# Kernel optimization log

Measured on AMD Instinct MI355X. Metric: run time of the kernel, lower is better.

Reference implementation:

```python
import jax, jax.numpy as jnp
import numpy as np

B, T, HID = 2, 2048, 2048
NH, NKV, D = 16, 4, 128
WIN = 512
ROPE_BASE = 10000.0
SCALE = D ** -0.5
EPS = 1e-12


def setup_inputs() -> dict:
    key = jax.random.key(0)
    ks = jax.random.split(key, 5)
    x = jax.random.normal(ks[0], (B, T, HID), dtype=jnp.float32)
    wq = jax.random.normal(ks[1], (HID, NH * D), dtype=jnp.float32) * 0.02
    wk = jax.random.normal(ks[2], (HID, NKV * D), dtype=jnp.float32) * 0.02
    wv = jax.random.normal(ks[3], (HID, NKV * D), dtype=jnp.float32) * 0.02
    wo = jax.random.normal(ks[4], (NH * D, HID), dtype=jnp.float32) * 0.02
    return {"x": x, "wq": wq, "wk": wk, "wv": wv, "wo": wo}


def _rope_tables(t, offset=0):
    inv_freq = 1.0 / (ROPE_BASE ** (jnp.arange(0, D, 2, dtype=jnp.float32) / D))
    pos = jnp.arange(offset, offset + t, dtype=jnp.float32)
    freqs = pos[:, None] * inv_freq[None, :]              # [t, D/2]
    cos = jnp.concatenate([jnp.cos(freqs), jnp.cos(freqs)], axis=-1)  # [t, D]
    sin = jnp.concatenate([jnp.sin(freqs), jnp.sin(freqs)], axis=-1)
    return cos, sin


def _apply_rope(x, cos, sin):
    # x: [B, H, T, D]; rotate-half formulation
    x1, x2 = jnp.split(x, 2, axis=-1)
    rot = jnp.concatenate([-x2, x1], axis=-1)
    return x * cos[None, None] + rot * sin[None, None]


def _l2norm(x):
    n = jnp.sqrt(jnp.sum(x * x, axis=-1, keepdims=True))
    return x / jnp.maximum(n, EPS)


def _forward(x, wq, wk, wv, wo):
    b, t, _ = x.shape
    q = (x @ wq).reshape(b, t, NH, D).transpose(0, 2, 1, 3)    # [B,H,T,D]
    k = (x @ wk).reshape(b, t, NKV, D).transpose(0, 2, 1, 3)   # [B,Hk,T,D]
    v = (x @ wv).reshape(b, t, NKV, D).transpose(0, 2, 1, 3)
    q = _l2norm(q)
    k = _l2norm(k)
    cos, sin = _rope_tables(t, offset=0)
    q = _apply_rope(q, cos, sin)
    k = _apply_rope(k, cos, sin)
    rep = NH // NKV
    k = jnp.repeat(k, rep, axis=1)                             # GQA repeat_interleave
    v = jnp.repeat(v, rep, axis=1)
    i = jnp.arange(t)
    allowed = (i[None, :] <= i[:, None]) & (i[None, :] > i[:, None] - WIN)  # [T,T]
    logits = jnp.einsum("bhid,bhjd->bhij", q, k) * SCALE
    logits = jnp.where(allowed[None, None], logits, -jnp.inf)
    attn = jax.nn.softmax(logits, axis=-1)
    out = jnp.einsum("bhij,bhjd->bhid", attn, v)
    out = out.transpose(0, 2, 1, 3).reshape(b, t, NH * D)
    return out @ wo


def reference(x, wq, wk, wv, wo):
    return _forward(x, wq, wk, wv, wo)
```

## Files before the change

kernel.cpp:

```cpp
#include <hip/hip_runtime.h>
#include <hip/hip_bf16.h>
#include <cstdint>

#define NHQ 16
#define NKVH 4
#define HDIM 128
#define WINSZ 512
#define TSEQ 2048
#define ATTN_SCALE 0.08838834764831845f

typedef __attribute__((ext_vector_type(8))) short s16x8;
typedef __attribute__((ext_vector_type(4))) float f32x4;

__device__ __forceinline__ void gload16(const void* g, void* lds) {
  __builtin_amdgcn_global_load_lds(
      (const __attribute__((address_space(1))) unsigned int*)g,
      (__attribute__((address_space(3))) unsigned int*)(uintptr_t)lds,
      16, 0, 0);
}

__device__ __forceinline__ f32x4 mfma16(s16x8 a, s16x8 b, f32x4 c) {
  return __builtin_amdgcn_mfma_f32_16x16x32_bf16(a, b, c, 0, 0, 0);
}

#define SBAR() asm volatile("s_barrier" ::: "memory")
#define VMCNT(n) asm volatile("s_waitcnt vmcnt(" #n ")" ::: "memory")
#define LGKM(n) asm volatile("s_waitcnt lgkmcnt(" #n ")" ::: "memory")

__global__ __launch_bounds__(256) void rope_tables_kernel(float* __restrict__ cosT,
                                                          float* __restrict__ sinT) {
  int idx = blockIdx.x * 256 + threadIdx.x;
  int t = idx >> 6, d2 = idx & 63;
  float inv = powf(10000.0f, -(float)d2 / 64.0f);
  float a = (float)t * inv;
  cosT[idx] = cosf(a);
  sinT[idx] = sinf(a);
}

__global__ __launch_bounds__(256) void cast_kernel(const float* __restrict__ in,
                                                   __bf16* __restrict__ out, int n4) {
  int i = blockIdx.x * 256 + threadIdx.x;
  if (i >= n4) return;
  float4 v = ((const float4*)in)[i];
  union { __bf16 h[4]; uint2 u; } pk;
  pk.h[0] = (__bf16)v.x; pk.h[1] = (__bf16)v.y; pk.h[2] = (__bf16)v.z; pk.h[3] = (__bf16)v.w;
  ((uint2*)out)[i] = pk.u;
}

__global__ __launch_bounds__(256) void transpose_cast(const float* __restrict__ in,
                                                      __bf16* __restrict__ out, int R, int C) {
  __shared__ float tile[32][33];
  int c0 = blockIdx.x * 32, r0 = blockIdx.y * 32;
  int tx = threadIdx.x, ty = threadIdx.y;
#pragma unroll
  for (int i = 0; i < 4; i++)
    tile[ty + i * 8][tx] = in[(size_t)(r0 + ty + i * 8) * C + c0 + tx];
  __syncthreads();
#pragma unroll
  for (int i = 0; i < 4; i++)
    out[(size_t)(c0 + ty + i * 8) * R + r0 + tx] = (__bf16)tile[tx][ty + i * 8];
}

__global__ __launch_bounds__(256) void vtrans(const __bf16* __restrict__ V,
                                              __bf16* __restrict__ VT) {
  __shared__ __bf16 t32[32][33];
  int bh = blockIdx.z;
  int t0 = blockIdx.y * 32, d0 = blockIdx.x * 32;
  const __bf16* src = V + (size_t)bh * TSEQ * HDIM;
  __bf16* dst = VT + (size_t)bh * HDIM * TSEQ;
  int tx = threadIdx.x, ty = threadIdx.y;
#pragma unroll
  for (int i = 0; i < 4; i++)
    t32[ty + i * 8][tx] = src[(size_t)(t0 + ty + i * 8) * HDIM + d0 + tx];
  __syncthreads();
#pragma unroll
  for (int i = 0; i < 4; i++)
    dst[(size_t)(d0 + ty + i * 8) * TSEQ + t0 + tx] = t32[tx][ty + i * 8];
}

template <int MODE>
__global__ __launch_bounds__(512, 2) void gemm8(const __bf16* __restrict__ A,
                                                const __bf16* __restrict__ Bt,
                                                float* __restrict__ Cf,
                                                __bf16* __restrict__ Qo, __bf16* __restrict__ Ko,
                                                __bf16* __restrict__ Vo, int M, int N, int K) {
  __shared__ __attribute__((aligned(16))) char Lds[2][65536];

  const int tid = threadIdx.x;
  const int w = tid >> 6, lane = tid & 63;
  const int wm = w >> 2, wn = w & 3;

  const int nbx = gridDim.x;
  const int nwg = nbx * gridDim.y;
  const int bid = blockIdx.y * nbx + blockIdx.x;
  const int q8 = nwg >> 3, r8 = nwg & 7;
  const int xcd = bid & 7, idx = bid >> 3;
  const int swz = (xcd < r8 ? xcd * (q8 + 1) : r8 * (q8 + 1) + (xcd - r8) * q8) + idx;
  const int bx = swz % nbx, by = swz / nbx;
  const int m0 = by * 256, n0 = bx * 256;

  const int ru = tid >> 3;
  const int cs = (tid & 7) ^ (ru & 7);
  const __bf16* gAs = A + (size_t)(m0 + ru) * K + cs * 8;
  const __bf16* gBs = Bt + (size_t)(n0 + ru) * K + cs * 8;

  auto stA = [&](int tt, int u) {
    gload16(gAs + (size_t)(64 * u) * K + tt * 64, Lds[tt & 1] + u * 8192 + w * 1024);
  };
  auto stB = [&](int tt, int u) {
    gload16(gBs + (size_t)(64 * u) * K + tt * 64, Lds[tt & 1] + 32768 + u * 8192 + w * 1024);
  };

  const int rowb = (lane & 15) * 128;
  const int cph0 = (((lane >> 4)) ^ (lane & 7)) * 16;
  const int cph1 = ((4 + (lane >> 4)) ^ (lane & 7)) * 16;
  const int Abase = wm * 16384;
  const int Bbase = 32768 + wn * 8192;

  f32x4 acc[8][4];
  f32x4 zero = {0.f, 0.f, 0.f, 0.f};
#pragma unroll
  for (int i = 0; i < 8; i++)
#pragma unroll
    for (int j = 0; j < 4; j++) acc[i][j] = zero;

  const int NT = K >> 6;

#pragma unroll
  for (int u = 0; u < 4; u++) stA(0, u);
#pragma unroll
  for (int u = 0; u < 4; u++) stB(0, u);
#pragma unroll
  for (int u = 0; u < 4; u++) stA(1, u);
#pragma unroll
  for (int u = 0; u < 4; u++) stB(1, u);
  VMCNT(8);
  SBAR();

  s16x8 fa[4][2], fb[4][2];

  for (int t = 0; t < NT; ++t) {
    const char* bs = Lds[t & 1];
    const bool more = (t + 2) < NT;

#pragma unroll
    for (int mi = 0; mi < 4; mi++) {
      fa[mi][0] = *(const s16x8*)(bs + Abase + mi * 2048 + rowb + cph0);
      fa[mi][1] = *(const s16x8*)(bs + Abase + mi * 2048 + rowb + cph1);
    }
#pragma unroll
    for (int ni = 0; ni < 2; ni++) {
      fb[ni][0] = *(const s16x8*)(bs + Bbase + ni * 2048 + rowb + cph0);
      fb[ni][1] = *(const s16x8*)(bs + Bbase + ni * 2048 + rowb + cph1);
    }
    SBAR();
    LGKM(0);
    __builtin_amdgcn_sched_barrier(0);
    __builtin_amdgcn_s_setprio(1);
#pragma unroll
    for (int mi = 0; mi < 4; mi++)
#pragma unroll
      for (int ni = 0; ni < 2; ni++)
#pragma unroll
        for (int kk = 0; kk < 2; kk++)
          acc[mi][ni] = mfma16(fa[mi][kk], fb[ni][kk], acc[mi][ni]);
    __builtin_amdgcn_s_setprio(0);
    SBAR();

#pragma unroll
    for (int ni = 2; ni < 4; ni++) {
      fb[ni][0] = *(const s16x8*)(bs + Bbase + ni * 2048 + rowb + cph0);
      fb[ni][1] = *(const s16x8*)(bs + Bbase + ni * 2048 + rowb + cph1);
    }
    if (more) { stA(t + 2, 0); stA(t + 2, 2); }
    SBAR();
    LGKM(0);
    __builtin_amdgcn_sched_barrier(0);
    __builtin_amdgcn_s_setprio(1);
#pragma unroll
    for (int mi = 0; mi < 4; mi++)
#pragma unroll
      for (int ni = 2; ni < 4; ni++)
#pragma unroll
        for (int kk = 0; kk < 2; kk++)
          acc[mi][ni] = mfma16(fa[mi][kk], fb[ni][kk], acc[mi][ni]);
    __builtin_amdgcn_s_setprio(0);
    SBAR();

#pragma unroll
    for (int mi = 0; mi < 4; mi++) {
      fa[mi][0] = *(const s16x8*)(bs + Abase + 8192 + mi * 2048 + rowb + cph0);
      fa[mi][1] = *(const s16x8*)(bs + Abase + 8192 + mi * 2048 + rowb + cph1);
    }
    if (more) { stB(t + 2, 0); stB(t + 2, 1); stB(t + 2, 2); stB(t + 2, 3); }
    SBAR();
    LGKM(0);
    __builtin_amdgcn_sched_barrier(0);
    __builtin_amdgcn_s_setprio(1);
#pragma unroll
    for (int mi = 0; mi < 4; mi++)
#pragma unroll
      for (int ni = 0; ni < 2; ni++)
#pragma unroll
        for (int kk = 0; kk < 2; kk++)
          acc[4 + mi][ni] = mfma16(fa[mi][kk], fb[ni][kk], acc[4 + mi][ni]);
    __builtin_amdgcn_s_setprio(0);
    SBAR();

    if (more) { stA(t + 2, 1); stA(t + 2, 3); }
    if (t + 2 < NT) {
      VMCNT(8);
    } else if (t + 1 < NT) {
      VMCNT(0);
    }
    SBAR();
    __builtin_amdgcn_s_setprio(1);
#pragma unroll
    for (int mi = 0; mi < 4; mi++)
#pragma unroll
      for (int ni = 2; ni < 4; ni++)
#pragma unroll
        for (int kk = 0; kk < 2; kk++)
          acc[4 + mi][ni] = mfma16(fa[mi][kk], fb[ni][kk], acc[4 + mi][ni]);
    __builtin_amdgcn_s_setprio(0);
    SBAR();
  }

#pragma unroll
  for (int mf = 0; mf < 8; mf++)
#pragma unroll
    for (int nf = 0; nf < 4; nf++) {
      int rbase = m0 + wm * 128 + mf * 16 + (lane >> 4) * 4;
      int col = n0 + wn * 64 + nf * 16 + (lane & 15);
#pragma unroll
      for (int r = 0; r < 4; r++) {
        int m = rbase + r;
        float v = acc[mf][nf][r];
        if constexpr (MODE == 0) {
          Cf[(size_t)m * N + col] = v;
        } else {
          int b = m >> 11, tq = m & 2047;
          __bf16 bv = (__bf16)v;
          if (col < 2048) {
            Qo[(((size_t)(b * NHQ + (col >> 7))) * TSEQ + tq) * HDIM + (col & 127)] = bv;
          } else if (col < 2560) {
            int c2 = col - 2048;
            Ko[(((size_t)(b * NKVH + (c2 >> 7))) * TSEQ + tq) * HDIM + (c2 & 127)] = bv;
          } else {
            int c2 = col - 2560;
            Vo[(((size_t)(b * NKVH + (c2 >> 7))) * TSEQ + tq) * HDIM + (c2 & 127)] = bv;
          }
        }
      }
    }
}

__global__ __launch_bounds__(256) void normrope(__bf16* __restrict__ Q, __bf16* __restrict__ Kk,
                                                const float* __restrict__ cosT,
                                                const float* __restrict__ sinT) {
  int w = threadIdx.x >> 6, lane = threadIdx.x & 63;
  int row = blockIdx.x / 5;
  int slot = (blockIdx.x % 5) * 4 + w;
  int b = row >> 11, t = row & 2047;
  __bf16* p;
  if (slot < 16)
    p = Q + (((size_t)(b * NHQ + slot)) * TSEQ + t) * HDIM;
  else
    p = Kk + (((size_t)(b * NKVH + (slot - 16))) * TSEQ + t) * HDIM;
  float x1 = (float)p[lane], x2 = (float)p[lane + 64];
  float ss = x1 * x1 + x2 * x2;
#pragma unroll
  for (int off = 32; off; off >>= 1) ss += __shfl_xor(ss, off);
  float inv = 1.0f / fmaxf(sqrtf(ss), 1e-12f);
  x1 *= inv;
  x2 *= inv;
  float c = cosT[t * 64 + lane], s = sinT[t * 64 + lane];
  p[lane] = (__bf16)(x1 * c - x2 * s);
  p[lane + 64] = (__bf16)(x2 * c + x1 * s);
}

__global__ __launch_bounds__(256) void attn_kernel(const __bf16* __restrict__ Qf,
                                                   const __bf16* __restrict__ Kf,
                                                   const __bf16* __restrict__ VTf,
                                                   __bf16* __restrict__ Ab) {
  __shared__ __attribute__((aligned(16))) char KlB[64 * 256];
  __shared__ __attribute__((aligned(16))) char VtB[128 * 128];
  __shared__ __attribute__((aligned(16))) char PlB[4 * 2048];
  int tid = threadIdx.x, w = tid >> 6, lane = tid & 63;
  int bid = blockIdx.x;
  int qt = bid & 31, h = (bid >> 5) & 15, b = bid >> 9;
  int qs = qt * 64;
  int kvh = h >> 2;
  const __bf16* Qb = Qf + ((size_t)(b * NHQ + h) * TSEQ) * HDIM;
  const __bf16* Kb = Kf + ((size_t)(b * NKVH + kvh) * TSEQ) * HDIM;
  const __bf16* VTb = VTf + ((size_t)(b * NKVH + kvh) * HDIM) * TSEQ;
  char* Pw = PlB + w * 2048;

  s16x8 aq[4];
  int qrow_f = qs + w * 16 + (lane & 15);
#pragma unroll
  for (int kb = 0; kb < 4; kb++)
    aq[kb] = *(const s16x8*)(Qb + (size_t)qrow_f * HDIM + kb * 32 + (lane >> 4) * 8);

  f32x4 acc[8];
  f32x4 zero = {0.f, 0.f, 0.f, 0.f};
#pragma unroll
  for (int db = 0; db < 8; db++) acc[db] = zero;
  float mrow[4], lrow[4];
#pragma unroll
  for (int r = 0; r < 4; r++) { mrow[r] = -1e30f; lrow[r] = 0.f; }

  int lo = qs - (WINSZ - 1);
  if (lo < 0) lo = 0;
  lo &= ~63;
  const int nt = ((qs + 64) - lo) >> 6;

  int4 kE[4], vE[4], kO[4], vO[4];

#define ATTN_LOAD(KR, VR, KS)                                                      \
  _Pragma("unroll") for (int i = 0; i < 4; i++) {                                  \
    KR[i] = *(const int4*)(Kb + (size_t)((KS) + (tid >> 4) + 16 * i) * HDIM +      \
                           (tid & 15) * 8);                                        \
    VR[i] = *(const int4*)(VTb + (size_t)((tid >> 3) + 32 * i) * TSEQ + (KS) +     \
                           (tid & 7) * 8);                                         \
  }

#define ATTN_WRITE(KR, VR)                                                         \
  _Pragma("unroll") for (int i = 0; i < 4; i++) {                                  \
    int jrow = (tid >> 4) + 16 * i;                                                \
    *(int4*)(KlB + jrow * 256 + (((tid & 15) * 16) ^ ((jrow & 7) << 4))) = KR[i];  \
    int drow = (tid >> 3) + 32 * i;                                                \
    *(int4*)(VtB + drow * 128 + (((tid & 7) * 16) ^ ((drow & 7) << 4))) = VR[i];   \
  }

#define ATTN_COMPUTE(KS)                                                           \
  {                                                                                \
    f32x4 sacc[4];                                                                 \
    _Pragma("unroll") for (int jb = 0; jb < 4; jb++) sacc[jb] = zero;              \
    _Pragma("unroll") for (int jb = 0; jb < 4; jb++) {                             \
      int key = jb * 16 + (lane & 15);                                             \
      _Pragma("unroll") for (int kb = 0; kb < 4; kb++) {                           \
        s16x8 bk = *(const s16x8*)(KlB + key * 256 +                               \
                                   ((kb * 64 + (lane >> 4) * 16) ^ ((key & 7) << 4))); \
        sacc[jb] = mfma16(aq[kb], bk, sacc[jb]);                                   \
      }                                                                            \
    }                                                                              \
    float scf[4];                                                                  \
    _Pragma("unroll") for (int r = 0; r < 4; r++) {                                \
      int qrow = qs + w * 16 + (lane >> 4) * 4 + r;                                \
      float sv[4]; bool av[4];                                                     \
      _Pragma("unroll") for (int jb = 0; jb < 4; jb++) {                           \
        int j = (KS) + jb * 16 + (lane & 15);                                      \
        av[jb] = (j <= qrow) && (j > qrow - WINSZ);                                \
        sv[jb] = sacc[jb][r] * ATTN_SCALE;                                         \
      }                                                                            \
      float mt = -1e30f;                                                           \
      _Pragma("unroll") for (int jb = 0; jb < 4; jb++)                             \
        mt = fmaxf(mt, av[jb] ? sv[jb] : -1e30f);                                  \
      _Pragma("unroll") for (int off = 1; off < 16; off <<= 1)                     \
        mt = fmaxf(mt, __shfl_xor(mt, off));                                       \
      float mn = fmaxf(mrow[r], mt);                                               \
      float pv_[4]; float ts = 0.f;                                                \
      _Pragma("unroll") for (int jb = 0; jb < 4; jb++) {                           \
        pv_[jb] = av[jb] ? __expf(sv[jb] - mn) : 0.f;                              \
        ts += pv_[jb];                                                             \
      }                                                                            \
      _Pragma("unroll") for (int off = 1; off < 16; off <<= 1)                     \
        ts += __shfl_xor(ts, off);                                                 \
      float sf = __expf(mrow[r] - mn);                                             \
      lrow[r] = lrow[r] * sf + ts;                                                 \
      mrow[r] = mn;                                                                \
      scf[r] = sf;                                                                 \
      int q = (lane >> 4) * 4 + r;                                                 \
      _Pragma("unroll") for (int jb = 0; jb < 4; jb++)                             \
        *(__bf16*)(Pw + q * 128 +                                                  \
                   (((jb * 16 + (lane & 15)) * 2) ^ ((q & 7) << 4))) = (__bf16)pv_[jb]; \
    }                                                                              \
    _Pragma("unroll") for (int db = 0; db < 8; db++) {                             \
      f32x4 tt = acc[db];                                                          \
      _Pragma("unroll") for (int r = 0; r < 4; r++) tt[r] *= scf[r];               \
      acc[db] = tt;                                                                \
    }                                                                              \
    s16x8 pa[2];                                                                   \
    _Pragma("unroll") for (int kb = 0; kb < 2; kb++) {                             \
      int q = lane & 15;                                                           \
      pa[kb] = *(const s16x8*)(Pw + q * 128 +                                      \
                               ((kb * 64 + (lane >> 4) * 16) ^ ((q & 7) << 4)));   \
    }                                                                              \
    _Pragma("unroll") for (int db = 0; db < 8; db++) {                             \
      int d = db * 16 + (lane & 15);                                               \
      _Pragma("unroll") for (int kb = 0; kb < 2; kb++) {                           \
        s16x8 bv = *(const s16x8*)(VtB + d * 128 +                                 \
                                   ((kb * 64 + (lane >> 4) * 16) ^ ((d & 7) << 4))); \
        acc[db] = mfma16(pa[kb], bv, acc[db]);                                     \
      }                                                                            \
    }                                                                              \
  }

  int ks = lo;
  ATTN_LOAD(kE, vE, ks);
  int it = 0;
  for (; it + 2 <= nt; it += 2) {
    ATTN_WRITE(kE, vE);
    ATTN_LOAD(kO, vO, ks + 64);
    __syncthreads();
    ATTN_COMPUTE(ks);
    __syncthreads();
    ks += 64;
    ATTN_WRITE(kO, vO);
    if (it + 2 < nt) ATTN_LOAD(kE, vE, ks + 64);
    __syncthreads();
    ATTN_COMPUTE(ks);
    __syncthreads();
    ks += 64;
  }
  if (it < nt) {
    ATTN_WRITE(kE, vE);
    __syncthreads();
    ATTN_COMPUTE(ks);
  }

#undef ATTN_LOAD
#undef ATTN_WRITE
#undef ATTN_COMPUTE

#pragma unroll
  for (int db = 0; db < 8; db++)
#pragma unroll
    for (int r = 0; r < 4; r++) {
      int qrow = qs + w * 16 + (lane >> 4) * 4 + r;
      float v = acc[db][r] / lrow[r];
      Ab[((size_t)(b * TSEQ + qrow)) * 2048 + h * HDIM + db * 16 + (lane & 15)] = (__bf16)v;
    }
}

extern "C" void kernel_launch(void* const* d_in, const int* in_sizes, int n_in,
                              void* d_out, int out_size, void* d_ws, size_t ws_size,
                              hipStream_t stream) {
  const float* x = (const float*)d_in[0];
  const float* wq = (const float*)d_in[1];
  const float* wk = (const float*)d_in[2];
  const float* wv = (const float*)d_in[3];
  const float* wo = (const float*)d_in[4];
  float* out = (float*)d_out;

  char* ws = (char*)d_ws;
  size_t off = 0;
  auto alloc = [&](size_t bytes) -> void* {
    void* p = ws + off;
    off += (bytes + 255) & ~(size_t)255;
    return p;
  };
  __bf16* Xb = (__bf16*)alloc((size_t)4096 * 2048 * 2);
  __bf16* Wqkvt = (__bf16*)alloc((size_t)3072 * 2048 * 2);
  __bf16* Wot = (__bf16*)alloc((size_t)2048 * 2048 * 2);
  __bf16* Q = (__bf16*)alloc((size_t)2 * NHQ * TSEQ * HDIM * 2);
  __bf16* Kb = (__bf16*)alloc((size_t)2 * NKVH * TSEQ * HDIM * 2);
  __bf16* Vb = (__bf16*)alloc((size_t)2 * NKVH * TSEQ * HDIM * 2);
  float* cosT = (float*)alloc((size_t)TSEQ * 64 * 4);
  float* sinT = (float*)alloc((size_t)TSEQ * 64 * 4);
  __bf16* Ab = Xb;
  __bf16* VT = Wqkvt;

  rope_tables_kernel<<<TSEQ * 64 / 256, 256, 0, stream>>>(cosT, sinT);
  cast_kernel<<<8192, 256, 0, stream>>>(x, Xb, 2097152);
  dim3 tb(32, 8);
  transpose_cast<<<dim3(64, 64), tb, 0, stream>>>(wq, Wqkvt, 2048, 2048);
  transpose_cast<<<dim3(16, 64), tb, 0, stream>>>(wk, Wqkvt + (size_t)2048 * 2048, 2048, 512);
  transpose_cast<<<dim3(16, 64), tb, 0, stream>>>(wv, Wqkvt + (size_t)2560 * 2048, 2048, 512);
  transpose_cast<<<dim3(64, 64), tb, 0, stream>>>(wo, Wot, 2048, 2048);

  gemm8<1><<<dim3(12, 16), 512, 0, stream>>>(Xb, Wqkvt, nullptr, Q, Kb, Vb, 4096, 3072, 2048);
  vtrans<<<dim3(4, 64, 2 * NKVH), tb, 0, stream>>>(Vb, VT);
  normrope<<<4096 * 5, 256, 0, stream>>>(Q, Kb, cosT, sinT);
  attn_kernel<<<2 * NHQ * (TSEQ / 64), 256, 0, stream>>>(Q, Kb, VT, Ab);
  gemm8<0><<<dim3(8, 16), 512, 0, stream>>>(Ab, Wot, out, nullptr, nullptr, nullptr, 4096, 2048,
                                            2048);
}
```

Before: 271.9 us.

## Share K/V tiles across GQA heads in one workgroup and drop V transpose kernel

The attention kernel now runs one 1024-thread workgroup per (batch, kv-head, q-tile), with 16 waves covering the 4 query heads that share a KV head. Each K/V tile is loaded once into LDS and reused by all four heads instead of being fetched four times. The separate V transpose kernel is removed: V is read row-major and scattered into the transposed LDS layout with scalar bf16 stores. This cuts global K/V traffic and one launch, but the scattered 2-byte LDS writes may cause bank conflicts, and 1024-thread blocks with larger LDS reduce scheduling flexibility and leave only 256 workgroups.

```diff
diff --git a/kernel.cpp b/kernel.cpp
--- a/kernel.cpp
+++ b/kernel.cpp
@@ -59,23 +59,6 @@
 #pragma unroll
   for (int i = 0; i < 4; i++)
     out[(size_t)(c0 + ty + i * 8) * R + r0 + tx] = (__bf16)tile[tx][ty + i * 8];
-}
-
-__global__ __launch_bounds__(256) void vtrans(const __bf16* __restrict__ V,
-                                              __bf16* __restrict__ VT) {
-  __shared__ __bf16 t32[32][33];
-  int bh = blockIdx.z;
-  int t0 = blockIdx.y * 32, d0 = blockIdx.x * 32;
-  const __bf16* src = V + (size_t)bh * TSEQ * HDIM;
-  __bf16* dst = VT + (size_t)bh * HDIM * TSEQ;
-  int tx = threadIdx.x, ty = threadIdx.y;
-#pragma unroll
-  for (int i = 0; i < 4; i++)
-    t32[ty + i * 8][tx] = src[(size_t)(t0 + ty + i * 8) * HDIM + d0 + tx];
-  __syncthreads();
-#pragma unroll
-  for (int i = 0; i < 4; i++)
-    dst[(size_t)(d0 + ty + i * 8) * TSEQ + t0 + tx] = t32[tx][ty + i * 8];
 }
 
 template <int MODE>
@@ -279,25 +262,26 @@
   p[lane + 64] = (__bf16)(x2 * c + x1 * s);
 }
 
-__global__ __launch_bounds__(256) void attn_kernel(const __bf16* __restrict__ Qf,
-                                                   const __bf16* __restrict__ Kf,
-                                                   const __bf16* __restrict__ VTf,
-                                                   __bf16* __restrict__ Ab) {
+__global__ __launch_bounds__(1024) void attn_kernel(const __bf16* __restrict__ Qf,
+                                                    const __bf16* __restrict__ Kf,
+                                                    const __bf16* __restrict__ Vf,
+                                                    __bf16* __restrict__ Ab) {
   __shared__ __attribute__((aligned(16))) char KlB[64 * 256];
   __shared__ __attribute__((aligned(16))) char VtB[128 * 128];
-  __shared__ __attribute__((aligned(16))) char PlB[4 * 2048];
+  __shared__ __attribute__((aligned(16))) char PlB[16 * 2048];
   int tid = threadIdx.x, w = tid >> 6, lane = tid & 63;
   int bid = blockIdx.x;
-  int qt = bid & 31, h = (bid >> 5) & 15, b = bid >> 9;
+  int qt = bid & 31, kvh = (bid >> 5) & 3, b = bid >> 7;
   int qs = qt * 64;
-  int kvh = h >> 2;
+  int h = kvh * 4 + (w >> 2);
+  int wr = w & 3;
   const __bf16* Qb = Qf + ((size_t)(b * NHQ + h) * TSEQ) * HDIM;
   const __bf16* Kb = Kf + ((size_t)(b * NKVH + kvh) * TSEQ) * HDIM;
-  const __bf16* VTb = VTf + ((size_t)(b * NKVH + kvh) * HDIM) * TSEQ;
+  const __bf16* Vb = Vf + ((size_t)(b * NKVH + kvh) * TSEQ) * HDIM;
   char* Pw = PlB + w * 2048;
 
   s16x8 aq[4];
-  int qrow_f = qs + w * 16 + (lane & 15);
+  int qrow_f = qs + wr * 16 + (lane & 15);
 #pragma unroll
   for (int kb = 0; kb < 4; kb++)
     aq[kb] = *(const s16x8*)(Qb + (size_t)qrow_f * HDIM + kb * 32 + (lane >> 4) * 8);
@@ -315,22 +299,25 @@
   lo &= ~63;
   const int nt = ((qs + 64) - lo) >> 6;
 
-  int4 kE[4], vE[4], kO[4], vO[4];
+  const int kjrow = tid >> 4, kkc = tid & 15;
+  const int vk = tid & 63, vd0 = (tid >> 6) * 8;
+
+  int4 kE, vE, kO, vO;
 
 #define ATTN_LOAD(KR, VR, KS)                                                      \
-  _Pragma("unroll") for (int i = 0; i < 4; i++) {                                  \
-    KR[i] = *(const int4*)(Kb + (size_t)((KS) + (tid >> 4) + 16 * i) * HDIM +      \
-                           (tid & 15) * 8);                                        \
-    VR[i] = *(const int4*)(VTb + (size_t)((tid >> 3) + 32 * i) * TSEQ + (KS) +     \
-                           (tid & 7) * 8);                                         \
+  {                                                                                \
+    KR = *(const int4*)(Kb + (size_t)((KS) + kjrow) * HDIM + kkc * 8);             \
+    VR = *(const int4*)(Vb + (size_t)((KS) + vk) * HDIM + vd0);                    \
   }
 
 #define ATTN_WRITE(KR, VR)                                                         \
-  _Pragma("unroll") for (int i = 0; i < 4; i++) {                                  \
-    int jrow = (tid >> 4) + 16 * i;                                                \
-    *(int4*)(KlB + jrow * 256 + (((tid & 15) * 16) ^ ((jrow & 7) << 4))) = KR[i];  \
-    int drow = (tid >> 3) + 32 * i;                                                \
-    *(int4*)(VtB + drow * 128 + (((tid & 7) * 16) ^ ((drow & 7) << 4))) = VR[i];   \
+  {                                                                                \
+    *(int4*)(KlB + kjrow * 256 + ((kkc * 16) ^ ((kjrow & 7) << 4))) = KR;          \
+    const __bf16* pv = (const __bf16*)&VR;                                         \
+    _Pragma("unroll") for (int e = 0; e < 8; e++) {                                \
+      int d = vd0 + e;                                                             \
+      *(__bf16*)(VtB + d * 128 + ((vk * 2) ^ ((d & 7) << 4))) = pv[e];             \
+    }                                                                              \
   }
 
 #define ATTN_COMPUTE(KS)                                                           \
@@ -347,7 +334,7 @@
     }                                                                              \
     float scf[4];                                                                  \
     _Pragma("unroll") for (int r = 0; r < 4; r++) {                                \
-      int qrow = qs + w * 16 + (lane >> 4) * 4 + r;                                \
+      int qrow = qs + wr * 16 + (lane >> 4) * 4 + r;                               \
       float sv[4]; bool av[4];                                                     \
       _Pragma("unroll") for (int jb = 0; jb < 4; jb++) {                           \
         int j = (KS) + jb * 16 + (lane & 15);                                      \
@@ -376,16 +363,16 @@
         *(__bf16*)(Pw + q * 128 +                                                  \
                    (((jb * 16 + (lane & 15)) * 2) ^ ((q & 7) << 4))) = (__bf16)pv_[jb]; \
     }                                                                              \
-    _Pragma("unroll") for (int db = 0; db < 8; db++) {                             \
-      f32x4 tt = acc[db];                                                          \
-      _Pragma("unroll") for (int r = 0; r < 4; r++) tt[r] *= scf[r];               \
-      acc[db] = tt;                                                                \
-    }                                                                              \
     s16x8 pa[2];                                                                   \
     _Pragma("unroll") for (int kb = 0; kb < 2; kb++) {                             \
       int q = lane & 15;                                                           \
       pa[kb] = *(const s16x8*)(Pw + q * 128 +                                      \
                                ((kb * 64 + (lane >> 4) * 16) ^ ((q & 7) << 4)));   \
+    }                                                                              \
+    _Pragma("unroll") for (int db = 0; db < 8; db++) {                             \
+      f32x4 tt = acc[db];                                                          \
+      _Pragma("unroll") for (int r = 0; r < 4; r++) tt[r] *= scf[r];               \
+      acc[db] = tt;                                                                \
     }                                                                              \
     _Pragma("unroll") for (int db = 0; db < 8; db++) {                             \
       int d = db * 16 + (lane & 15);                                               \
@@ -428,7 +415,7 @@
   for (int db = 0; db < 8; db++)
 #pragma unroll
     for (int r = 0; r < 4; r++) {
-      int qrow = qs + w * 16 + (lane >> 4) * 4 + r;
+      int qrow = qs + wr * 16 + (lane >> 4) * 4 + r;
       float v = acc[db][r] / lrow[r];
       Ab[((size_t)(b * TSEQ + qrow)) * 2048 + h * HDIM + db * 16 + (lane & 15)] = (__bf16)v;
     }
@@ -460,7 +447,6 @@
   float* cosT = (float*)alloc((size_t)TSEQ * 64 * 4);
   float* sinT = (float*)alloc((size_t)TSEQ * 64 * 4);
   __bf16* Ab = Xb;
-  __bf16* VT = Wqkvt;
 
   rope_tables_kernel<<<TSEQ * 64 / 256, 256, 0, stream>>>(cosT, sinT);
   cast_kernel<<<8192, 256, 0, stream>>>(x, Xb, 2097152);
@@ -471,9 +457,8 @@
   transpose_cast<<<dim3(64, 64), tb, 0, stream>>>(wo, Wot, 2048, 2048);
 
   gemm8<1><<<dim3(12, 16), 512, 0, stream>>>(Xb, Wqkvt, nullptr, Q, Kb, Vb, 4096, 3072, 2048);
-  vtrans<<<dim3(4, 64, 2 * NKVH), tb, 0, stream>>>(Vb, VT);
   normrope<<<4096 * 5, 256, 0, stream>>>(Q, Kb, cosT, sinT);
-  attn_kernel<<<2 * NHQ * (TSEQ / 64), 256, 0, stream>>>(Q, Kb, VT, Ab);
+  attn_kernel<<<2 * NKVH * (TSEQ / 64), 1024, 0, stream>>>(Q, Kb, Vb, Ab);
   gemm8<0><<<dim3(8, 16), 512, 0, stream>>>(Ab, Wot, out, nullptr, nullptr, nullptr, 4096, 2048,
                                             2048);
 }
```

After: 255.5 us. -6.1%, faster.
